# Kernel tuning notes

Measured on AMD Instinct MI355X. Metric: run time of the kernel, lower is better.

## Reference

```python
import jax, jax.numpy as jnp
import numpy as np

B, S, D = 2, 2048, 4096
H, KVH, HD = 32, 8, 128
REPEATS = H // KVH
SCALE = HD ** -0.5


def setup_inputs() -> dict:
    key = jax.random.key(0)
    ks = jax.random.split(key, 5)
    x = jax.random.normal(ks[0], (B, S, D), dtype=jnp.float32)
    # RoPE tables: shape (S, HD//2)
    t = jnp.arange(S, dtype=jnp.float32)
    inv_freq = 1.0 / (10000.0 ** (jnp.arange(0, HD, 2, dtype=jnp.float32) / HD))
    freqs = jnp.outer(t, inv_freq)
    freqs_cos = jnp.cos(freqs)
    freqs_sin = jnp.sin(freqs)
    # causal additive mask [B, S, S]
    i = jnp.arange(S)
    causal = jnp.where(i[:, None] >= i[None, :], 0.0, -1e9).astype(jnp.float32)
    mask = jnp.broadcast_to(causal[None], (B, S, S))
    positions = jnp.arange(S, dtype=jnp.int32)
    w_std = 0.02
    wq = jax.random.normal(ks[1], (D, H * HD), dtype=jnp.float32) * w_std
    wk = jax.random.normal(ks[2], (D, KVH * HD), dtype=jnp.float32) * w_std
    wv = jax.random.normal(ks[3], (D, KVH * HD), dtype=jnp.float32) * w_std
    wo = jax.random.normal(ks[4], (H * HD, D), dtype=jnp.float32) * w_std
    return dict(x=x, freqs_cos=freqs_cos, freqs_sin=freqs_sin, mask=mask,
                wq=wq, wk=wk, wv=wv, wo=wo, positions=positions)


def _apply_rope(t, fc, fs):
    # t: [B, S, h, HD]; interleaved (real, imag) pairs along last dim
    tr = t.reshape(t.shape[:-1] + (HD // 2, 2))
    r, i = tr[..., 0], tr[..., 1]
    c = fc[None, :, None, :]  # [1, S, 1, HD//2]
    s = fs[None, :, None, :]
    out_r = r * c - i * s
    out_i = r * s + i * c
    return jnp.stack([out_r, out_i], axis=-1).reshape(t.shape)


def reference(x, freqs_cos, freqs_sin, mask, wq, wk, wv, wo, positions):
    bsz, seqlen, _ = x.shape
    xq = (x @ wq).reshape(bsz, seqlen, H, HD)
    xk = (x @ wk).reshape(bsz, seqlen, KVH, HD)
    xv = (x @ wv).reshape(bsz, seqlen, KVH, HD)
    xq = _apply_rope(xq, freqs_cos, freqs_sin)
    xk = _apply_rope(xk, freqs_cos, freqs_sin)
    # GQA: repeat_interleave over kv-head dim
    key = jnp.repeat(xk, REPEATS, axis=2)   # [B, S, H, HD]
    value = jnp.repeat(xv, REPEATS, axis=2)
    q = xq.transpose(0, 2, 1, 3)            # [B, H, S, HD]
    k = key.transpose(0, 2, 1, 3)
    v = value.transpose(0, 2, 1, 3)
    scores = jnp.einsum('bhqd,bhkd->bhqk', q, k) * SCALE
    scores = scores + mask[:, None, :, :]
    probs = jax.nn.softmax(scores.astype(jnp.float32), axis=-1)
    out = jnp.einsum('bhqk,bhkd->bhqd', probs, v)
    out = out.transpose(0, 2, 1, 3).reshape(bsz, seqlen, H * HD)
    out = jnp.nan_to_num(out)
    return out @ wo
```

## Files before the change

kernel.cpp:

```cpp
#include <hip/hip_runtime.h>

typedef unsigned short ushort_t;
typedef unsigned int uint32;

#define SCALE_F 0.08838834764831845f

using bf16x8 = __attribute__((ext_vector_type(8))) short;
using f32x4  = __attribute__((ext_vector_type(4))) float;
using u32x4  = __attribute__((ext_vector_type(4))) uint32;
using u32x2  = __attribute__((ext_vector_type(2))) uint32;

__device__ __forceinline__ float b2f(ushort_t h) {
  union { uint32 u; float f; } v; v.u = ((uint32)h) << 16; return v.f;
}
__device__ __forceinline__ ushort_t f2b(float f) {
  union { float f; uint32 u; } v; v.f = f;
  uint32 r = (v.u + 0x7fffu + ((v.u >> 16) & 1u)) >> 16;
  return (ushort_t)r;
}
__device__ __forceinline__ uint32 pk2(float a, float b) {
  union { float f; uint32 u; } x, y; x.f = a; y.f = b;
  return __builtin_amdgcn_perm(y.u + 0x8000u, x.u + 0x8000u, 0x07060302u);
}
__device__ __forceinline__ void gl2lds16(const void* g, void* l) {
  __builtin_amdgcn_global_load_lds(
      (const __attribute__((address_space(1))) uint32*)g,
      (__attribute__((address_space(3))) uint32*)l, 16, 0, 0);
}
__device__ __forceinline__ void fence_mem() { asm volatile("" ::: "memory"); }
__device__ __forceinline__ void bar() {
  fence_mem();
  __builtin_amdgcn_s_barrier();
  fence_mem();
}
template <int N>
__device__ __forceinline__ void waitvm() {
  if constexpr (N == 6) asm volatile("s_waitcnt vmcnt(6)" ::: "memory");
  else if constexpr (N == 8) asm volatile("s_waitcnt vmcnt(8)" ::: "memory");
  else asm volatile("s_waitcnt vmcnt(0)" ::: "memory");
}

constexpr int LDP = 40;


__global__ __launch_bounds__(256)
void xconv(const float* __restrict__ x, ushort_t* __restrict__ xb) {
  size_t i = ((size_t)blockIdx.x * 256 + threadIdx.x) * 8;
  f32x4 a = *(const f32x4*)&x[i];
  f32x4 b = *(const f32x4*)&x[i + 4];
  u32x4 p = {pk2(a[0], a[1]), pk2(a[2], a[3]), pk2(b[0], b[1]), pk2(b[2], b[3])};
  *(u32x4*)&xb[i] = p;
}

__global__ __launch_bounds__(256)
void wtrans(const float* __restrict__ src, ushort_t* __restrict__ dst, int N) {
  __shared__ float ts[32][33];
  int n0 = blockIdx.x * 32, k0 = blockIdx.y * 32;
  int tid = threadIdx.x;
  {
    int r = tid >> 3, c4 = (tid & 7) * 4;
    f32x4 v = *(const f32x4*)&src[(size_t)(k0 + r) * N + n0 + c4];
    ts[r][c4 + 0] = v[0]; ts[r][c4 + 1] = v[1];
    ts[r][c4 + 2] = v[2]; ts[r][c4 + 3] = v[3];
  }
  __syncthreads();
  int rn = tid >> 3, ck = (tid & 7) * 4;
  u32x2 p = {pk2(ts[ck + 0][rn], ts[ck + 1][rn]),
             pk2(ts[ck + 2][rn], ts[ck + 3][rn])};
  *(u32x2*)&dst[(size_t)(n0 + rn) * 4096 + k0 + ck] = p;
}


template <int ROWS, int AMODE>
__device__ __forceinline__ void stage_region(const ushort_t* __restrict__ P,
                                             int row0, int k, ushort_t* lds,
                                             int tid) {
#pragma unroll
  for (int i = 0; i < ROWS / 128; ++i) {
    int s = i * 512 + tid;
    int r = s >> 2, c = s & 3;
    int qq = c ^ ((r >> 1) & 3);
    const ushort_t* ga;
    if (AMODE == 0) {
      ga = P + (size_t)(row0 + r) * 4096 + k + qq * 8;
    } else {
      int m = row0 + r, bb = m >> 11, ss = m & 2047;
      int kk = k + qq * 8;
      int hh = kk >> 7, dg = (kk >> 5) & 3;
      ga = P + ((((size_t)(bb * 32 + hh) * 32 + (ss >> 6)) * 4 + dg) * 64 +
                (ss & 63)) * 32 + (kk & 31);
    }
    gl2lds16(ga, lds + ((size_t)(i * 512 + (tid & 448))) * 8);
  }
}

template <int BM, int VMC, int AMODE>
__device__ __forceinline__ void gemm8_core(const ushort_t* __restrict__ A,
                                           const ushort_t* __restrict__ B,
                                           int m0, int n0, ushort_t* As,
                                           ushort_t* Bs, f32x4 (*acc)[4]) {
  constexpr int FR = BM / 32;
  constexpr int ASZ = BM * 32;
  constexpr int BSZ = 256 * 32;
  const int tid = threadIdx.x;
  const int lane = tid & 63, q = lane >> 4, cl = lane & 15;
  const int w = tid >> 6, wrow = w >> 2, wcol = w & 3;

  auto phase = [&](int pl, int qc, auto issue, bool dovm) {
    bf16x8 af[FR], bfr[2];
    const ushort_t* ap = As + pl * ASZ;
    const ushort_t* bp = Bs + pl * BSZ;
#pragma unroll
    for (int fr = 0; fr < FR; ++fr) {
      int rr = wrow * (BM / 2) + fr * 16 + cl;
      af[fr] = *(const bf16x8*)&ap[rr * 32 + (q ^ ((rr >> 1) & 3)) * 8];
    }
#pragma unroll
    for (int fb = 0; fb < 2; ++fb) {
      int rn = wcol * 64 + qc * 32 + fb * 16 + cl;
      bfr[fb] = *(const bf16x8*)&bp[rn * 32 + (q ^ ((rn >> 1) & 3)) * 8];
    }
    issue();
    bar();
    __builtin_amdgcn_s_setprio(1);
#pragma unroll
    for (int fr = 0; fr < FR; ++fr)
#pragma unroll
      for (int fb = 0; fb < 2; ++fb)
        acc[fr][qc * 2 + fb] = __builtin_amdgcn_mfma_f32_16x16x32_bf16(
            af[fr], bfr[fb], acc[fr][qc * 2 + fb], 0, 0, 0);
    __builtin_amdgcn_s_setprio(0);
    if (dovm) waitvm<VMC>();
    bar();
  };

  stage_region<BM, AMODE>(A, m0, 0, As + 0 * ASZ, tid);
  stage_region<256, 0>(B, n0, 0, Bs + 0 * BSZ, tid);
  stage_region<BM, AMODE>(A, m0, 32, As + 1 * ASZ, tid);
  stage_region<256, 0>(B, n0, 32, Bs + 1 * BSZ, tid);
  stage_region<BM, AMODE>(A, m0, 64, As + 2 * ASZ, tid);
  stage_region<256, 0>(B, n0, 64, Bs + 2 * BSZ, tid);
  waitvm<VMC>();
  bar();

  for (int it = 0; it < 32; ++it) {
    int k1h = it * 128 + 96;
    int t2 = it * 128 + 128; if (t2 > 4032) t2 = 4032;
    int t3 = it * 128 + 192; if (t3 > 4032) t3 = 4032;
    phase(0, 0, [&] { stage_region<BM, AMODE>(A, m0, k1h, As + 3 * ASZ, tid); }, false);
    phase(0, 1, [&] { stage_region<256, 0>(B, n0, k1h, Bs + 3 * BSZ, tid); }, true);
    phase(1, 0, [&] { stage_region<BM, AMODE>(A, m0, t2, As + 0 * ASZ, tid); }, false);
    phase(1, 1, [&] { stage_region<256, 0>(B, n0, t2, Bs + 0 * BSZ, tid); }, true);
    phase(2, 0, [&] { stage_region<BM, AMODE>(A, m0, t2 + 32, As + 1 * ASZ, tid); }, false);
    phase(2, 1, [&] { stage_region<256, 0>(B, n0, t2 + 32, Bs + 1 * BSZ, tid); }, true);
    phase(3, 0, [&] { stage_region<BM, AMODE>(A, m0, t3, As + 2 * ASZ, tid); }, false);
    phase(3, 1, [&] { stage_region<256, 0>(B, n0, t3, Bs + 2 * BSZ, tid); }, true);
  }
  waitvm<0>();
  bar();
}

__global__ __launch_bounds__(512, 2)
void qkv_gemm8(const ushort_t* __restrict__ xb, const ushort_t* __restrict__ wt,
               const float* __restrict__ fc, const float* __restrict__ fs,
               ushort_t* __restrict__ qg, ushort_t* __restrict__ kg,
               ushort_t* __restrict__ vg) {
  __shared__ ushort_t As[4 * 128 * 32];
  __shared__ ushort_t Bs[4 * 256 * 32];
  int bid = blockIdx.x;
  int swz = (bid & 7) * 96 + (bid >> 3);
  int tx = swz / 32, ty = swz % 32;
  int n0 = tx * 256, m0 = ty * 128;
  f32x4 acc[4][4] = {};
  gemm8_core<128, 6, 0>(xb, wt, m0, n0, As, Bs, acc);
  const int tid = threadIdx.x;
  const int lane = tid & 63, q = lane >> 4, cl = lane & 15;
  const int w = tid >> 6, wrow = w >> 2, wcol = w & 3;
  if (n0 < 5120) {
    ushort_t* dst = (n0 < 4096) ? qg : kg;
    int NHH = (n0 < 4096) ? 32 : 8;
    int nc = (n0 < 4096) ? n0 : n0 - 4096;
    for (int fr = 0; fr < 4; ++fr)
      for (int fcc = 0; fcc < 4; ++fcc)
        for (int rg = 0; rg < 4; ++rg) {
          int row = m0 + wrow * 64 + fr * 16 + q * 4 + rg;
          int b = row >> 11, s = row & 2047;
          int col = nc + wcol * 64 + fcc * 16 + cl;
          int hh = col >> 7, d = col & 127;
          float val = acc[fr][fcc][rg];
          float par = __shfl_xor(val, 1);
          float cf = fc[(size_t)s * 64 + (d >> 1)];
          float sf = fs[(size_t)s * 64 + (d >> 1)];
          float o = val * cf + par * ((d & 1) ? sf : -sf);
          size_t off =
              ((((size_t)(b * NHH + hh) * 32 + (s >> 6)) * 4 + (d >> 5)) * 64 +
               (s & 63)) * 32 + (d & 31);
          dst[off] = f2b(o);
        }
  } else {
    int nc = n0 - 5120;
    for (int fr = 0; fr < 4; ++fr)
      for (int fcc = 0; fcc < 4; ++fcc)
        for (int rg = 0; rg < 4; ++rg) {
          int row = m0 + wrow * 64 + fr * 16 + q * 4 + rg;
          int b = row >> 11, s = row & 2047;
          int col = nc + wcol * 64 + fcc * 16 + cl;
          int kvh = col >> 7, d = col & 127;
          size_t off =
              ((((size_t)(b * 8 + kvh) * 32 + (s >> 6)) * 2 + ((s >> 5) & 1)) *
                   128 + d) * 32 + (s & 31);
          vg[off] = f2b(acc[fr][fcc][rg]);
        }
  }
}

__global__ __launch_bounds__(512, 2)
void out_gemm8(const ushort_t* __restrict__ attn,
               const ushort_t* __restrict__ wot, float* __restrict__ out) {
  __shared__ ushort_t As[4 * 256 * 32];
  __shared__ ushort_t Bs[4 * 256 * 32];
  int bid = blockIdx.x;
  int swz = (bid & 7) * 32 + (bid >> 3);
  int tx = swz >> 4, ty = swz & 15;
  int n0 = tx * 256, m0 = ty * 256;
  f32x4 acc[8][4] = {};
  gemm8_core<256, 8, 1>(attn, wot, m0, n0, As, Bs, acc);
  const int tid = threadIdx.x;
  const int lane = tid & 63, q = lane >> 4, cl = lane & 15;
  const int w = tid >> 6, wrow = w >> 2, wcol = w & 3;
  for (int fr = 0; fr < 8; ++fr)
    for (int fcc = 0; fcc < 4; ++fcc)
      for (int rg = 0; rg < 4; ++rg) {
        int row = m0 + wrow * 128 + fr * 16 + q * 4 + rg;
        int col = n0 + wcol * 64 + fcc * 16 + cl;
        out[(size_t)row * 4096 + col] = acc[fr][fcc][rg];
      }
}


template <int AMODE>
__device__ __forceinline__ void gemm_core_cvt(const void* __restrict__ A,
                                              const float* __restrict__ B, int K,
                                              int NB, int m0, int nb0,
                                              ushort_t* As, ushort_t* Bs,
                                              f32x4 acc[4][4]) {
  int tid = threadIdx.x;
  int lane = tid & 63, w = tid >> 6, q = lane >> 4, cl = lane & 15;
  int wr = (w >> 1) * 64, wc = (w & 1) * 64;
  int ar = tid >> 1, ah = tid & 1;
  int bn = tid & 127, bh = tid >> 7;
  for (int k0 = 0; k0 < K; k0 += 32) {
    __syncthreads();
    if (AMODE == 0) {
      const float* ap = &((const float*)A)[(size_t)(m0 + ar) * K + k0 + ah * 16];
      f32x4 a0 = *(const f32x4*)(ap + 0);
      f32x4 a1 = *(const f32x4*)(ap + 4);
      f32x4 a2 = *(const f32x4*)(ap + 8);
      f32x4 a3 = *(const f32x4*)(ap + 12);
      u32x4 p0 = {pk2(a0[0], a0[1]), pk2(a0[2], a0[3]), pk2(a1[0], a1[1]),
                  pk2(a1[2], a1[3])};
      u32x4 p1 = {pk2(a2[0], a2[1]), pk2(a2[2], a2[3]), pk2(a3[0], a3[1]),
                  pk2(a3[2], a3[3])};
      *(u32x4*)&As[ar * LDP + ah * 16] = p0;
      *(u32x4*)&As[ar * LDP + ah * 16 + 8] = p1;
    } else {
      int m = m0 + ar, bb = m >> 11, s = m & 2047;
      int k = k0 + ah * 16;
      int hh = k >> 7, dg = (k >> 5) & 3, el = k & 31;
      size_t off =
          ((((size_t)(bb * 32 + hh) * 32 + (s >> 6)) * 4 + dg) * 64 +
           (s & 63)) * 32 + el;
      const ushort_t* ap = (const ushort_t*)A + off;
      u32x4 v0 = *(const u32x4*)(ap + 0);
      u32x4 v1 = *(const u32x4*)(ap + 8);
      *(u32x4*)&As[ar * LDP + ah * 16] = v0;
      *(u32x4*)&As[ar * LDP + ah * 16 + 8] = v1;
    }
    {
      float bv[16];
#pragma unroll
      for (int j = 0; j < 16; ++j)
        bv[j] = B[(size_t)(k0 + bh * 16 + j) * NB + nb0 + bn];
      u32x4 p0 = {pk2(bv[0], bv[1]), pk2(bv[2], bv[3]), pk2(bv[4], bv[5]),
                  pk2(bv[6], bv[7])};
      u32x4 p1 = {pk2(bv[8], bv[9]), pk2(bv[10], bv[11]), pk2(bv[12], bv[13]),
                  pk2(bv[14], bv[15])};
      *(u32x4*)&Bs[bn * LDP + bh * 16] = p0;
      *(u32x4*)&Bs[bn * LDP + bh * 16 + 8] = p1;
    }
    __syncthreads();
    bf16x8 af[4], bfr[4];
    for (int rt = 0; rt < 4; ++rt)
      af[rt] = *(const bf16x8*)&As[(wr + rt * 16 + cl) * LDP + q * 8];
    for (int ct = 0; ct < 4; ++ct)
      bfr[ct] = *(const bf16x8*)&Bs[(wc + ct * 16 + cl) * LDP + q * 8];
    for (int rt = 0; rt < 4; ++rt)
      for (int ct = 0; ct < 4; ++ct)
        acc[rt][ct] = __builtin_amdgcn_mfma_f32_16x16x32_bf16(
            af[rt], bfr[ct], acc[rt][ct], 0, 0, 0);
  }
}

__global__ __launch_bounds__(256, 3)
void qkv_gemm_cvt(const float* __restrict__ x, const float* __restrict__ wq,
                  const float* __restrict__ wk, const float* __restrict__ wv,
                  const float* __restrict__ fc, const float* __restrict__ fs,
                  ushort_t* __restrict__ qg, ushort_t* __restrict__ kg,
                  ushort_t* __restrict__ vg) {
  __shared__ ushort_t As[128 * LDP];
  __shared__ ushort_t Bs[128 * LDP];
  int n0 = blockIdx.x * 128, m0 = blockIdx.y * 128;
  const float* Bp; int NB, nc;
  if (n0 < 4096)      { Bp = wq; NB = 4096; nc = n0; }
  else if (n0 < 5120) { Bp = wk; NB = 1024; nc = n0 - 4096; }
  else                { Bp = wv; NB = 1024; nc = n0 - 5120; }
  f32x4 acc[4][4] = {};
  gemm_core_cvt<0>(x, Bp, 4096, NB, m0, nc, As, Bs, acc);
  int tid = threadIdx.x;
  int lane = tid & 63, w = tid >> 6, q = lane >> 4, cl = lane & 15;
  int wr = (w >> 1) * 64, wc = (w & 1) * 64;
  if (n0 < 5120) {
    ushort_t* dst = (n0 < 4096) ? qg : kg;
    int NHH = (n0 < 4096) ? 32 : 8;
    for (int rt = 0; rt < 4; ++rt)
      for (int ct = 0; ct < 4; ++ct)
        for (int rg = 0; rg < 4; ++rg) {
          int row = m0 + wr + rt * 16 + q * 4 + rg;
          int b = row >> 11, s = row & 2047;
          int col = nc + wc + ct * 16 + cl;
          int hh = col >> 7, d = col & 127;
          float val = acc[rt][ct][rg];
          float par = __shfl_xor(val, 1);
          float cf = fc[(size_t)s * 64 + (d >> 1)];
          float sf = fs[(size_t)s * 64 + (d >> 1)];
          float o = val * cf + par * ((d & 1) ? sf : -sf);
          size_t off =
              ((((size_t)(b * NHH + hh) * 32 + (s >> 6)) * 4 + (d >> 5)) * 64 +
               (s & 63)) * 32 + (d & 31);
          dst[off] = f2b(o);
        }
  } else {
    for (int rt = 0; rt < 4; ++rt)
      for (int ct = 0; ct < 4; ++ct)
        for (int rg = 0; rg < 4; ++rg) {
          int row = m0 + wr + rt * 16 + q * 4 + rg;
          int b = row >> 11, s = row & 2047;
          int col = nc + wc + ct * 16 + cl;
          int kvh = col >> 7, d = col & 127;
          size_t off =
              ((((size_t)(b * 8 + kvh) * 32 + (s >> 6)) * 2 + ((s >> 5) & 1)) *
                   128 + d) * 32 + (s & 31);
          vg[off] = f2b(acc[rt][ct][rg]);
        }
  }
}

__global__ __launch_bounds__(256, 3)
void out_gemm_cvt(const ushort_t* __restrict__ attn,
                  const float* __restrict__ wo, float* __restrict__ out) {
  __shared__ ushort_t As[128 * LDP];
  __shared__ ushort_t Bs[128 * LDP];
  int n0 = blockIdx.x * 128, m0 = blockIdx.y * 128;
  f32x4 acc[4][4] = {};
  gemm_core_cvt<1>(attn, wo, 4096, 4096, m0, n0, As, Bs, acc);
  int tid = threadIdx.x;
  int lane = tid & 63, w = tid >> 6, q = lane >> 4, cl = lane & 15;
  int wr = (w >> 1) * 64, wc = (w & 1) * 64;
  for (int rt = 0; rt < 4; ++rt)
    for (int ct = 0; ct < 4; ++ct)
      for (int rg = 0; rg < 4; ++rg) {
        int row = m0 + wr + rt * 16 + q * 4 + rg;
        int col = n0 + wc + ct * 16 + cl;
        out[(size_t)row * 4096 + col] = acc[rt][ct][rg];
      }
}

__device__ __forceinline__ void stage_tile(const ushort_t* src, ushort_t* dst,
                                           int tid) {
  for (int cc = 0; cc < 4; ++cc)
    gl2lds16(src + (size_t)(cc * 256 + tid) * 8,
             dst + (size_t)(cc * 256 + (tid & 192)) * 8);
}

__global__ __launch_bounds__(256, 2)
void flash_attn(ushort_t* __restrict__ qg, const ushort_t* __restrict__ kg,
                const ushort_t* __restrict__ vg) {
  __shared__ ushort_t Ks[2][8192];
  __shared__ ushort_t Vs[2][8192];
  __shared__ ushort_t Ps[4096];
  int tid = threadIdx.x;
  int w = tid >> 6, lane = tid & 63, q = lane >> 4, cl = lane & 15;
  int idx = blockIdx.x;
  int qb = 31 - (idx >> 6);
  int bh = idx & 63;
  int b = bh >> 5, h = bh & 31, kvh = h >> 2;

  ushort_t* qt = qg + ((size_t)(b * 32 + h) * 32 + qb) * 8192;
  bf16x8 aq[4];
  for (int ks = 0; ks < 4; ++ks)
    aq[ks] = *(const bf16x8*)&qt[ks * 2048 + (w * 16 + cl) * 32 + q * 8];

  const ushort_t* kb = kg + ((size_t)(b * 8 + kvh) * 32) * 8192;
  const ushort_t* vb = vg + ((size_t)(b * 8 + kvh) * 32) * 8192;
  stage_tile(kb, Ks[0], tid);
  stage_tile(vb, Vs[0], tid);

  f32x4 oacc[8] = {};
  float m_i[4], l_i[4];
  for (int rg = 0; rg < 4; ++rg) { m_i[rg] = -3e30f; l_i[rg] = 0.f; }

  for (int jb = 0; jb <= qb; ++jb) {
    __syncthreads();
    int cur = jb & 1, nxt = (jb + 1) & 1;
    int jn = (jb + 1 > qb) ? qb : jb + 1;
    stage_tile(kb + (size_t)jn * 8192, Ks[nxt], tid);
    stage_tile(vb + (size_t)jn * 8192, Vs[nxt], tid);
    f32x4 sacc[4] = {};
    for (int ks = 0; ks < 4; ++ks)
      for (int ct = 0; ct < 4; ++ct) {
        bf16x8 bk =
            *(const bf16x8*)&Ks[cur][ks * 2048 + (ct * 16 + cl) * 32 + q * 8];
        sacc[ct] =
            __builtin_amdgcn_mfma_f32_16x16x32_bf16(aq[ks], bk, sacc[ct], 0, 0, 0);
      }
    float pv[4][4], mt[4];
    bool diag = (jb == qb);
    for (int rg = 0; rg < 4; ++rg) mt[rg] = -3e30f;
    for (int ct = 0; ct < 4; ++ct)
      for (int rg = 0; rg < 4; ++rg) {
        float sv = sacc[ct][rg] * SCALE_F;
        if (diag) {
          int rrow = w * 16 + q * 4 + rg;
          int ccol = ct * 16 + cl;
          if (ccol > rrow) sv = -3e30f;
        }
        pv[ct][rg] = sv;
        mt[rg] = fmaxf(mt[rg], sv);
      }
    for (int off = 1; off < 16; off <<= 1)
      for (int rg = 0; rg < 4; ++rg)
        mt[rg] = fmaxf(mt[rg], __shfl_xor(mt[rg], off));
    float alpha[4], rs[4];
    for (int rg = 0; rg < 4; ++rg) {
      float mn = fmaxf(m_i[rg], mt[rg]);
      alpha[rg] = __expf(m_i[rg] - mn);
      m_i[rg] = mn;
      rs[rg] = 0.f;
    }
    for (int ct = 0; ct < 4; ++ct)
      for (int rg = 0; rg < 4; ++rg) {
        float p = __expf(pv[ct][rg] - m_i[rg]);
        pv[ct][rg] = p;
        rs[rg] += p;
      }
    for (int off = 1; off < 16; off <<= 1)
      for (int rg = 0; rg < 4; ++rg) rs[rg] += __shfl_xor(rs[rg], off);
    for (int rg = 0; rg < 4; ++rg) l_i[rg] = l_i[rg] * alpha[rg] + rs[rg];
    for (int nt = 0; nt < 8; ++nt)
      for (int rg = 0; rg < 4; ++rg) oacc[nt][rg] *= alpha[rg];
    for (int ct = 0; ct < 4; ++ct)
      for (int rg = 0; rg < 4; ++rg) {
        int off_ = w * 1024 + (ct >> 1) * 512 + (q * 4 + rg) * 32 +
                   (ct & 1) * 16 + cl;
        Ps[off_] = f2b(pv[ct][rg]);
      }
    for (int ks2 = 0; ks2 < 2; ++ks2) {
      bf16x8 pa = *(const bf16x8*)&Ps[w * 1024 + ks2 * 512 + cl * 32 + q * 8];
      for (int nt = 0; nt < 8; ++nt) {
        bf16x8 bv =
            *(const bf16x8*)&Vs[cur][ks2 * 4096 + (nt * 16 + cl) * 32 + q * 8];
        oacc[nt] =
            __builtin_amdgcn_mfma_f32_16x16x32_bf16(pa, bv, oacc[nt], 0, 0, 0);
      }
    }
  }
  for (int nt = 0; nt < 8; ++nt)
    for (int rg = 0; rg < 4; ++rg) {
      float v = oacc[nt][rg] / l_i[rg];
      int rowt = w * 16 + q * 4 + rg;
      int d = nt * 16 + cl;
      qt[(d >> 5) * 2048 + rowt * 32 + (d & 31)] = f2b(v);
    }
}

extern "C" void kernel_launch(void* const* d_in, const int* in_sizes, int n_in,
                              void* d_out, int out_size, void* d_ws,
                              size_t ws_size, hipStream_t stream) {
  const float* x  = (const float*)d_in[0];
  const float* fc = (const float*)d_in[1];
  const float* fs = (const float*)d_in[2];
  const float* wq = (const float*)d_in[4];
  const float* wk = (const float*)d_in[5];
  const float* wv = (const float*)d_in[6];
  const float* wo = (const float*)d_in[7];
  ushort_t* ws = (ushort_t*)d_ws;

  ushort_t* qg = ws;
  ushort_t* kg = qg + (size_t)4096 * 4096;
  ushort_t* vg = kg + (size_t)4096 * 1024;

  if (ws_size >= (size_t)128 * 1024 * 1024) {
    ushort_t* wt = vg + (size_t)4096 * 1024;
    ushort_t* xb = wt + (size_t)6144 * 4096;
    xconv<<<8192, 256, 0, stream>>>(x, xb);
    wtrans<<<dim3(128, 128), 256, 0, stream>>>(wq, wt, 4096);
    wtrans<<<dim3(32, 128), 256, 0, stream>>>(wk, wt + (size_t)4096 * 4096, 1024);
    wtrans<<<dim3(32, 128), 256, 0, stream>>>(wv, wt + (size_t)5120 * 4096, 1024);
    qkv_gemm8<<<768, 512, 0, stream>>>(xb, wt, fc, fs, qg, kg, vg);
    wtrans<<<dim3(128, 128), 256, 0, stream>>>(wo, xb, 4096);
    flash_attn<<<2048, 256, 0, stream>>>(qg, kg, vg);
    out_gemm8<<<256, 512, 0, stream>>>(qg, xb, (float*)d_out);
  } else {
    qkv_gemm_cvt<<<dim3(48, 32), 256, 0, stream>>>(x, wq, wk, wv, fc, fs, qg,
                                                   kg, vg);
    flash_attn<<<2048, 256, 0, stream>>>(qg, kg, vg);
    out_gemm_cvt<<<dim3(32, 32), 256, 0, stream>>>(qg, wo, (float*)d_out);
  }
}
```

Measured before the change: 839.1 us.

## Restructure bf16 GEMM main loop into one full k-slice per barrier pair

The GEMM core loop now handles a whole 32-wide k-slice per step: it reads all four B fragments, issues both A and B stages for the slice three steps ahead, and runs the full set of MFMAs between two barriers. Previously each slice was split into two half-phases, with A and B staged separately and vmcnt waits only every other phase. This halves the number of barriers and LDS-read rounds per k-slice. In exchange it raises register pressure from the extra B fragments and makes each step wait on more outstanding loads.

```diff
diff --git a/kernel.cpp b/kernel.cpp
--- a/kernel.cpp
+++ b/kernel.cpp
@@ -94,67 +94,59 @@
   }
 }
 
-template <int BM, int VMC, int AMODE>
-__device__ __forceinline__ void gemm8_core(const ushort_t* __restrict__ A,
-                                           const ushort_t* __restrict__ B,
-                                           int m0, int n0, ushort_t* As,
-                                           ushort_t* Bs, f32x4 (*acc)[4]) {
+template <int BM, int AMODE>
+__device__ __forceinline__ void gemm8p_core(const ushort_t* __restrict__ A,
+                                            const ushort_t* __restrict__ B,
+                                            int m0, int n0, ushort_t* As,
+                                            ushort_t* Bs, f32x4 (*acc)[4]) {
   constexpr int FR = BM / 32;
   constexpr int ASZ = BM * 32;
   constexpr int BSZ = 256 * 32;
+  constexpr int SPP = BM / 128 + 2;
+  constexpr int VMC = 2 * SPP;
   const int tid = threadIdx.x;
   const int lane = tid & 63, q = lane >> 4, cl = lane & 15;
   const int w = tid >> 6, wrow = w >> 2, wcol = w & 3;
 
-  auto phase = [&](int pl, int qc, auto issue, bool dovm) {
-    bf16x8 af[FR], bfr[2];
+  auto stage_pair = [&](int pl, int k) {
+    stage_region<BM, AMODE>(A, m0, k, As + pl * ASZ, tid);
+    stage_region<256, 0>(B, n0, k, Bs + pl * BSZ, tid);
+  };
+
+  stage_pair(0, 0);
+  stage_pair(1, 32);
+  stage_pair(2, 64);
+  waitvm<VMC>();
+  bar();
+
+  for (int t = 0; t < 128; ++t) {
+    int pl = t & 3;
+    int kf = (t + 3) * 32; if (kf > 4064) kf = 4064;
     const ushort_t* ap = As + pl * ASZ;
     const ushort_t* bp = Bs + pl * BSZ;
+    bf16x8 af[FR], bfr[4];
 #pragma unroll
     for (int fr = 0; fr < FR; ++fr) {
       int rr = wrow * (BM / 2) + fr * 16 + cl;
       af[fr] = *(const bf16x8*)&ap[rr * 32 + (q ^ ((rr >> 1) & 3)) * 8];
     }
 #pragma unroll
-    for (int fb = 0; fb < 2; ++fb) {
-      int rn = wcol * 64 + qc * 32 + fb * 16 + cl;
+    for (int fb = 0; fb < 4; ++fb) {
+      int rn = wcol * 64 + fb * 16 + cl;
       bfr[fb] = *(const bf16x8*)&bp[rn * 32 + (q ^ ((rn >> 1) & 3)) * 8];
     }
-    issue();
+    stage_pair((t + 3) & 3, kf);
     bar();
     __builtin_amdgcn_s_setprio(1);
 #pragma unroll
     for (int fr = 0; fr < FR; ++fr)
 #pragma unroll
-      for (int fb = 0; fb < 2; ++fb)
-        acc[fr][qc * 2 + fb] = __builtin_amdgcn_mfma_f32_16x16x32_bf16(
-            af[fr], bfr[fb], acc[fr][qc * 2 + fb], 0, 0, 0);
+      for (int fb = 0; fb < 4; ++fb)
+        acc[fr][fb] = __builtin_amdgcn_mfma_f32_16x16x32_bf16(
+            af[fr], bfr[fb], acc[fr][fb], 0, 0, 0);
     __builtin_amdgcn_s_setprio(0);
-    if (dovm) waitvm<VMC>();
+    waitvm<VMC>();
     bar();
-  };
-
-  stage_region<BM, AMODE>(A, m0, 0, As + 0 * ASZ, tid);
-  stage_region<256, 0>(B, n0, 0, Bs + 0 * BSZ, tid);
-  stage_region<BM, AMODE>(A, m0, 32, As + 1 * ASZ, tid);
-  stage_region<256, 0>(B, n0, 32, Bs + 1 * BSZ, tid);
-  stage_region<BM, AMODE>(A, m0, 64, As + 2 * ASZ, tid);
-  stage_region<256, 0>(B, n0, 64, Bs + 2 * BSZ, tid);
-  waitvm<VMC>();
-  bar();
-
-  for (int it = 0; it < 32; ++it) {
-    int k1h = it * 128 + 96;
-    int t2 = it * 128 + 128; if (t2 > 4032) t2 = 4032;
-    int t3 = it * 128 + 192; if (t3 > 4032) t3 = 4032;
-    phase(0, 0, [&] { stage_region<BM, AMODE>(A, m0, k1h, As + 3 * ASZ, tid); }, false);
-    phase(0, 1, [&] { stage_region<256, 0>(B, n0, k1h, Bs + 3 * BSZ, tid); }, true);
-    phase(1, 0, [&] { stage_region<BM, AMODE>(A, m0, t2, As + 0 * ASZ, tid); }, false);
-    phase(1, 1, [&] { stage_region<256, 0>(B, n0, t2, Bs + 0 * BSZ, tid); }, true);
-    phase(2, 0, [&] { stage_region<BM, AMODE>(A, m0, t2 + 32, As + 1 * ASZ, tid); }, false);
-    phase(2, 1, [&] { stage_region<256, 0>(B, n0, t2 + 32, Bs + 1 * BSZ, tid); }, true);
-    phase(3, 0, [&] { stage_region<BM, AMODE>(A, m0, t3, As + 2 * ASZ, tid); }, false);
-    phase(3, 1, [&] { stage_region<256, 0>(B, n0, t3, Bs + 2 * BSZ, tid); }, true);
   }
   waitvm<0>();
   bar();
@@ -172,7 +164,7 @@
   int tx = swz / 32, ty = swz % 32;
   int n0 = tx * 256, m0 = ty * 128;
   f32x4 acc[4][4] = {};
-  gemm8_core<128, 6, 0>(xb, wt, m0, n0, As, Bs, acc);
+  gemm8p_core<128, 0>(xb, wt, m0, n0, As, Bs, acc);
   const int tid = threadIdx.x;
   const int lane = tid & 63, q = lane >> 4, cl = lane & 15;
   const int w = tid >> 6, wrow = w >> 2, wcol = w & 3;
@@ -224,7 +216,7 @@
   int tx = swz >> 4, ty = swz & 15;
   int n0 = tx * 256, m0 = ty * 256;
   f32x4 acc[8][4] = {};
-  gemm8_core<256, 8, 1>(attn, wot, m0, n0, As, Bs, acc);
+  gemm8p_core<256, 1>(attn, wot, m0, n0, As, Bs, acc);
   const int tid = threadIdx.x;
   const int lane = tid & 63, q = lane >> 4, cl = lane & 15;
   const int w = tid >> 6, wrow = w >> 2, wcol = w & 3;
```

New measurement: 786.9 us. -6.2%, faster.
